# Kernel tuning notes

Hardware: AMD Instinct MI355X
Metric: run time of the kernel (lower is better)

Reference implementation:

```python
import jax, jax.numpy as jnp
import numpy as np

MARGIN = 1.0
N, D = 8192, 128
NUM_CLASSES = 1024


def setup_inputs() -> dict:
    key = jax.random.key(0)
    k1, k2, k3 = jax.random.split(key, 3)
    a = jax.random.normal(k1, (N, D), dtype=jnp.float32)
    b = jax.random.normal(k2, (N, D), dtype=jnp.float32)
    # L2-normalize embeddings (standard for metric learning; keeps exp() stable)
    a = a / jnp.linalg.norm(a, axis=1, keepdims=True)
    b = b / jnp.linalg.norm(b, axis=1, keepdims=True)
    labels = jax.random.randint(k3, (N,), 0, NUM_CLASSES, dtype=jnp.int64 if jax.config.jax_enable_x64 else jnp.int32)
    return {"a": a, "b": b, "labels": labels}


def reference(a, b, labels):
    # S[i, j] = a_i . b_j  -- full pairwise similarity, one GEMM
    S = a @ b.T  # [N, N]
    same = labels[:, None] == labels[None, :]  # [N, N]
    eye = jnp.eye(labels.shape[0], dtype=bool)
    pos_mask = same & ~eye          # ordered positive pairs (i != j, same label)
    neg_mask = ~same                # ordered negative pairs (labels differ)
    # V[i] = sum_k in neg(i) exp(margin + S[i, k])
    V = jnp.sum(jnp.where(neg_mask, jnp.exp(MARGIN + S), 0.0), axis=1)  # [N]
    # per positive pair (i, j): max(log(V_i + V_j) - S_ij, 0)^2
    hinge = jnp.maximum(jnp.log(V[:, None] + V[None, :]) - S, 0.0)
    comp = jnp.where(pos_mask, hinge * hinge, 0.0)
    num_pos = jnp.sum(pos_mask)
    loss = jnp.sum(comp) / (2.0 * num_pos.astype(S.dtype))
    return loss
```

## Files before the change

### kernel.cpp

```cpp
#include <hip/hip_runtime.h>

#define NN 8192
#define DD 128
#define MARGINF 1.0f
#define MAXCLS 64
#define NCHUNK 8
#define LOG2E 1.4426950408889634f
#define E1    2.718281828459045f

typedef __attribute__((ext_vector_type(8))) short bf16x8;
typedef __attribute__((ext_vector_type(4))) float f32x4;

#if __has_builtin(__builtin_amdgcn_exp2f)
#define EXP2F(x) __builtin_amdgcn_exp2f(x)
#else
#define EXP2F(x) exp2f(x)
#endif

__device__ __forceinline__ void load16_lds(const unsigned short* g, unsigned short* l) {
    __builtin_amdgcn_global_load_lds(
        (const __attribute__((address_space(1))) unsigned int*)g,
        (__attribute__((address_space(3))) unsigned int*)l,
        16, 0, 0);
}

__device__ __forceinline__ unsigned short f2bf(float x) {
    unsigned u = __float_as_uint(x);
    u = (u + 0x7FFFu + ((u >> 16) & 1u)) >> 16;
    return (unsigned short)u;
}

__global__ __launch_bounds__(256) void ml_convert_kernel(
    const float* __restrict__ a, const float* __restrict__ b,
    const int* __restrict__ labels,
    unsigned short* __restrict__ abf, unsigned short* __restrict__ bbf,
    int* __restrict__ cnt, int* __restrict__ list)
{
    int t = blockIdx.x * 256 + threadIdx.x;
    const float* src = a;
    unsigned short* dst = abf;
    int idx = t;
    float scale = LOG2E;
    if (t >= 262144) { src = b; dst = bbf; idx = t - 262144; scale = 1.0f; }
    float4 v = ((const float4*)src)[idx];
    ushort4 o;
    o.x = f2bf(v.x * scale); o.y = f2bf(v.y * scale);
    o.z = f2bf(v.z * scale); o.w = f2bf(v.w * scale);
    ((ushort4*)dst)[idx] = o;

    if (t < NN) {
        int c = labels[t];
        int p = atomicAdd(&cnt[c], 1);
        if (p < MAXCLS) list[c * MAXCLS + p] = t;
    }
}

__global__ __launch_bounds__(256, 2) void ml_vsum_gemm_kernel(
    const unsigned short* __restrict__ abf, const unsigned short* __restrict__ bbf,
    float* __restrict__ Vp)
{
    __shared__ unsigned short As[128 * DD];
    __shared__ unsigned short Bs[2][64 * DD];
    __shared__ float red[2][64];

    const int tid  = threadIdx.x;
    const int lane = tid & 63;
    const int wv   = tid >> 6;
    const int row0 = blockIdx.y * 128;
    const int j0   = blockIdx.x * 1024;

    const int lr = lane >> 4;
    const int p  = lane & 15;
    const int m  = lane & 15;
    const int q  = lane >> 4;
    const int xr = m & 7;

#pragma unroll
    for (int i = 0; i < 8; i++) {
        int rb = wv * 32 + i * 4;
        int r  = rb + lr;
        int cc = p ^ (r & 7);
        load16_lds(&abf[(size_t)(row0 + r) * DD + cc * 8], &As[rb * DD]);
    }
#pragma unroll
    for (int i = 0; i < 4; i++) {
        int rb = wv * 16 + i * 4;
        int r  = rb + lr;
        int cc = p ^ (r & 7);
        load16_lds(&bbf[(size_t)(j0 + r) * DD + cc * 8], &Bs[0][rb * DD]);
    }
#pragma unroll
    for (int i = 0; i < 4; i++) {
        int rb = wv * 16 + i * 4;
        int r  = rb + lr;
        int cc = p ^ (r & 7);
        load16_lds(&bbf[(size_t)(j0 + 64 + r) * DD + cc * 8], &Bs[1][rb * DD]);
    }
    __syncthreads();

    const int wi = (wv >> 1) * 64;
    const int wj = (wv & 1) * 32;

    bf16x8 afr[4][4];
#pragma unroll
    for (int ti = 0; ti < 4; ti++)
#pragma unroll
        for (int ks = 0; ks < 4; ks++) {
            int r   = wi + ti * 16 + m;
            int pos = (ks * 4 + q) ^ xr;
            afr[ti][ks] = *(const bf16x8*)(&As[r * DD + pos * 8]);
        }

    float rs[4][4];
#pragma unroll
    for (int ti = 0; ti < 4; ti++)
#pragma unroll
        for (int rg = 0; rg < 4; rg++) rs[ti][rg] = 0.f;

    const f32x4 zero = {0.f, 0.f, 0.f, 0.f};

#pragma unroll 2
    for (int jt = 0; jt < 16; jt++) {
        const int pb = jt & 1;
        f32x4 acc[4][2];
#pragma unroll
        for (int ti = 0; ti < 4; ti++)
#pragma unroll
            for (int tj = 0; tj < 2; tj++) acc[ti][tj] = zero;

#pragma unroll
        for (int ks = 0; ks < 4; ks++) {
            bf16x8 bfr[2];
#pragma unroll
            for (int tj = 0; tj < 2; tj++) {
                int r   = wj + tj * 16 + m;
                int pos = (ks * 4 + q) ^ xr;
                bfr[tj] = *(const bf16x8*)(&Bs[pb][r * DD + pos * 8]);
            }
#pragma unroll
            for (int ti = 0; ti < 4; ti++)
#pragma unroll
                for (int tj = 0; tj < 2; tj++)
                    acc[ti][tj] = __builtin_amdgcn_mfma_f32_16x16x32_bf16(afr[ti][ks], bfr[tj], acc[ti][tj], 0, 0, 0);
        }

#pragma unroll
        for (int ti = 0; ti < 4; ti++)
#pragma unroll
            for (int tj = 0; tj < 2; tj++) {
                f32x4 c = acc[ti][tj];
                rs[ti][0] += EXP2F(c[0]);
                rs[ti][1] += EXP2F(c[1]);
                rs[ti][2] += EXP2F(c[2]);
                rs[ti][3] += EXP2F(c[3]);
            }

        __syncthreads();
        if (jt < 14) {
            int jb = j0 + (jt + 2) * 64;
#pragma unroll
            for (int i = 0; i < 4; i++) {
                int rb = wv * 16 + i * 4;
                int r  = rb + lr;
                int cc = p ^ (r & 7);
                load16_lds(&bbf[(size_t)(jb + r) * DD + cc * 8], &Bs[pb][rb * DD]);
            }
        }
    }

#pragma unroll
    for (int ti = 0; ti < 4; ti++)
#pragma unroll
        for (int rg = 0; rg < 4; rg++) {
            float v = rs[ti][rg];
            v += __shfl_xor(v, 1);
            v += __shfl_xor(v, 2);
            v += __shfl_xor(v, 4);
            v += __shfl_xor(v, 8);
            rs[ti][rg] = v;
        }

    if ((wv & 1) == 1 && m == 0) {
#pragma unroll
        for (int ti = 0; ti < 4; ti++)
#pragma unroll
            for (int rg = 0; rg < 4; rg++)
                red[wv >> 1][ti * 16 + q * 4 + rg] = rs[ti][rg];
    }
    __syncthreads();
    if ((wv & 1) == 0 && m == 0) {
#pragma unroll
        for (int ti = 0; ti < 4; ti++)
#pragma unroll
            for (int rg = 0; rg < 4; rg++) {
                int rloc = ti * 16 + q * 4 + rg;
                Vp[(size_t)blockIdx.x * NN + row0 + wi + rloc] = rs[ti][rg] + red[wv >> 1][rloc];
            }
    }
}

__global__ __launch_bounds__(256) void ml_pairs_kernel(
    const float* __restrict__ a, const float* __restrict__ b,
    const int* __restrict__ cnt, const int* __restrict__ list,
    const float* __restrict__ Vp,
    float* __restrict__ classLoss, int* __restrict__ classCnt,
    unsigned int* __restrict__ done, float* __restrict__ out)
{
    __shared__ int   mem[MAXCLS];
    __shared__ float sumExp[MAXCLS];
    __shared__ float Vadj[MAXCLS];
    __shared__ float Sc[MAXCLS * MAXCLS];
    __shared__ float ps[4];
    __shared__ int   cs[4];
    __shared__ double dred[4];
    __shared__ long long cred[4];

    const int c   = blockIdx.x;
    const int tid = threadIdx.x;
    int mc = cnt[c];
    if (mc > MAXCLS) mc = MAXCLS;

    float vsum = 0.f;
    if (tid < mc) {
        int r = list[c * MAXCLS + tid];
        mem[tid] = r;
#pragma unroll
        for (int jc = 0; jc < NCHUNK; jc++) vsum += Vp[(size_t)jc * NN + r];
    }
    if (tid < MAXCLS) sumExp[tid] = 0.f;
    __syncthreads();

    const int g = tid >> 4;
    const int l = tid & 15;
    const int tot1 = mc * mc;
    for (int pp = g; pp < tot1; pp += 16) {
        int i = pp / mc;
        int j = pp - i * mc;
        int ri = mem[i], rj = mem[j];
        const float4* ar = (const float4*)(a + (size_t)ri * DD) + l * 2;
        const float4* br = (const float4*)(b + (size_t)rj * DD) + l * 2;
        float4 a0 = ar[0], a1 = ar[1];
        float4 b0 = br[0], b1 = br[1];
        float s = 0.f;
        s = fmaf(a0.x, b0.x, s); s = fmaf(a0.y, b0.y, s);
        s = fmaf(a0.z, b0.z, s); s = fmaf(a0.w, b0.w, s);
        s = fmaf(a1.x, b1.x, s); s = fmaf(a1.y, b1.y, s);
        s = fmaf(a1.z, b1.z, s); s = fmaf(a1.w, b1.w, s);
        s += __shfl_xor(s, 1);
        s += __shfl_xor(s, 2);
        s += __shfl_xor(s, 4);
        s += __shfl_xor(s, 8);
        if (l == 0) {
            Sc[i * MAXCLS + j] = s;
            atomicAdd(&sumExp[i], __expf(s));
        }
    }
    __syncthreads();

    if (tid < mc) Vadj[tid] = E1 * (vsum - sumExp[tid]);
    __syncthreads();

    float partial = 0.f;
    int   count   = 0;
    for (int pp = tid; pp < tot1; pp += 256) {
        int i = pp / mc;
        int j = pp - i * mc;
        if (i != j) {
            float h = fmaxf(logf(Vadj[i] + Vadj[j]) - Sc[i * MAXCLS + j], 0.f);
            partial += h * h;
            count++;
        }
    }
    for (int off = 32; off > 0; off >>= 1) {
        partial += __shfl_down(partial, off);
        count   += __shfl_down(count, off);
    }
    const int lane = tid & 63, wv = tid >> 6;
    if (lane == 0) { ps[wv] = partial; cs[wv] = count; }
    __syncthreads();

    if (tid == 0) {
        float tot = ps[0] + ps[1] + ps[2] + ps[3];
        int   ct  = cs[0] + cs[1] + cs[2] + cs[3];
        atomicExch(&classLoss[c], tot);
        atomicExch(&classCnt[c], ct);
    }
    __syncthreads();

    if (tid == 0) ps[0] = (float)atomicAdd(done, 1u);
    __syncthreads();
    if ((unsigned)ps[0] == 1023u) {
        double dls = 0.0;
        long long dct = 0;
        for (int k = tid; k < 1024; k += 256) {
            dls += (double)atomicAdd(&classLoss[k], 0.0f);
            dct += (long long)atomicAdd(&classCnt[k], 0);
        }
        for (int off = 32; off > 0; off >>= 1) {
            dls += __shfl_down(dls, off);
            dct += __shfl_down(dct, off);
        }
        if (lane == 0) { dred[wv] = dls; cred[wv] = dct; }
        __syncthreads();
        if (tid == 0) {
            double ls = dred[0] + dred[1] + dred[2] + dred[3];
            long long np = cred[0] + cred[1] + cred[2] + cred[3];
            out[0] = (float)(ls / (2.0 * (double)np));
        }
    }
}

extern "C" void kernel_launch(void* const* d_in, const int* in_sizes, int n_in,
                              void* d_out, int out_size, void* d_ws, size_t ws_size,
                              hipStream_t stream)
{
    const float* a      = (const float*)d_in[0];
    const float* b      = (const float*)d_in[1];
    const int*   labels = (const int*)d_in[2];
    float* out = (float*)d_out;

    char* ws = (char*)d_ws;
    unsigned short* abf = (unsigned short*)ws;
    unsigned short* bbf = (unsigned short*)(ws + 2097152);
    char*     base2     = ws + 4194304;
    int*      cnt       = (int*)(base2);
    unsigned* done      = (unsigned*)(base2 + 4096);
    float*    classLoss = (float*)(base2 + 8192);
    int*      classCnt  = (int*)(base2 + 12288);
    int*      list      = (int*)(base2 + 16384);
    float*    Vp        = (float*)(base2 + 278528);

    hipMemsetAsync(base2, 0, 4100, stream);

    ml_convert_kernel<<<2048, 256, 0, stream>>>(a, b, labels, abf, bbf, cnt, list);

    dim3 g(NCHUNK, NN / 128);
    ml_vsum_gemm_kernel<<<g, 256, 0, stream>>>(abf, bbf, Vp);

    ml_pairs_kernel<<<1024, 256, 0, stream>>>(a, b, cnt, list, Vp, classLoss, classCnt, done, out);
}
```

Measured before the change: 113.6 us.

## Fuse three kernels into one persistent kernel with grid barriers

Merges the convert, V-sum GEMM and per-class pair kernels into a single launch of 512 blocks, separated by software grid barriers built on atomics and fences. The shared-memory buffers of the phases are overlaid in a union, and each block handles two classes in the final phase. The goal is to remove the gaps and launch overhead between kernels. In exchange it depends on all 512 blocks being resident at once (two per CU), else the spin barrier deadlocks, and the pair phase now runs on half as many blocks.

```diff
diff --git a/kernel.cpp b/kernel.cpp
--- a/kernel.cpp
+++ b/kernel.cpp
@@ -2,9 +2,9 @@
 
 #define NN 8192
 #define DD 128
-#define MARGINF 1.0f
 #define MAXCLS 64
 #define NCHUNK 8
+#define GRID 512
 #define LOG2E 1.4426950408889634f
 #define E1    2.718281828459045f
 
@@ -17,6 +17,14 @@
 #define EXP2F(x) exp2f(x)
 #endif
 
+#if __has_builtin(__builtin_amdgcn_fence)
+#define FENCE_REL() __builtin_amdgcn_fence(__ATOMIC_RELEASE, "agent")
+#define FENCE_ACQ() __builtin_amdgcn_fence(__ATOMIC_ACQUIRE, "agent")
+#else
+#define FENCE_REL() __threadfence()
+#define FENCE_ACQ() __threadfence()
+#endif
+
 __device__ __forceinline__ void load16_lds(const unsigned short* g, unsigned short* l) {
     __builtin_amdgcn_global_load_lds(
         (const __attribute__((address_space(1))) unsigned int*)g,
@@ -30,266 +38,291 @@
     return (unsigned short)u;
 }
 
-__global__ __launch_bounds__(256) void ml_convert_kernel(
+__device__ __forceinline__ void grid_barrier(unsigned int* slot) {
+    FENCE_REL();
+    __syncthreads();
+    if (threadIdx.x == 0) {
+        atomicAdd(slot, 1u);
+        while (atomicAdd(slot, 0u) < (unsigned)GRID)
+            __builtin_amdgcn_s_sleep(2);
+    }
+    __syncthreads();
+    FENCE_ACQ();
+}
+
+__global__ __launch_bounds__(256, 2) void ml_mega_kernel(
     const float* __restrict__ a, const float* __restrict__ b,
     const int* __restrict__ labels,
     unsigned short* __restrict__ abf, unsigned short* __restrict__ bbf,
-    int* __restrict__ cnt, int* __restrict__ list)
+    int* __restrict__ cnt, int* __restrict__ list, float* __restrict__ Vp,
+    float* __restrict__ classLoss, int* __restrict__ classCnt,
+    unsigned int* __restrict__ bar, unsigned int* __restrict__ done,
+    float* __restrict__ out)
 {
-    int t = blockIdx.x * 256 + threadIdx.x;
-    const float* src = a;
-    unsigned short* dst = abf;
-    int idx = t;
-    float scale = LOG2E;
-    if (t >= 262144) { src = b; dst = bbf; idx = t - 262144; scale = 1.0f; }
-    float4 v = ((const float4*)src)[idx];
-    ushort4 o;
-    o.x = f2bf(v.x * scale); o.y = f2bf(v.y * scale);
-    o.z = f2bf(v.z * scale); o.w = f2bf(v.w * scale);
-    ((ushort4*)dst)[idx] = o;
-
-    if (t < NN) {
-        int c = labels[t];
-        int p = atomicAdd(&cnt[c], 1);
-        if (p < MAXCLS) list[c * MAXCLS + p] = t;
-    }
-}
-
-__global__ __launch_bounds__(256, 2) void ml_vsum_gemm_kernel(
-    const unsigned short* __restrict__ abf, const unsigned short* __restrict__ bbf,
-    float* __restrict__ Vp)
-{
-    __shared__ unsigned short As[128 * DD];
-    __shared__ unsigned short Bs[2][64 * DD];
-    __shared__ float red[2][64];
+    __shared__ union {
+        struct {
+            unsigned short As[128 * DD];
+            unsigned short Bs[2][64 * DD];
+            float red[2][64];
+        } g;
+        struct {
+            float Sc[MAXCLS * MAXCLS];
+            int   mem[MAXCLS];
+            float sumExp[MAXCLS];
+            float vadj[MAXCLS];
+            float ps[4];  int cs[4];
+            double dred[4];  long long cred[4];
+        } p;
+    } sh;
 
     const int tid  = threadIdx.x;
     const int lane = tid & 63;
     const int wv   = tid >> 6;
-    const int row0 = blockIdx.y * 128;
-    const int j0   = blockIdx.x * 1024;
-
-    const int lr = lane >> 4;
-    const int p  = lane & 15;
-    const int m  = lane & 15;
-    const int q  = lane >> 4;
-    const int xr = m & 7;
-
-#pragma unroll
-    for (int i = 0; i < 8; i++) {
-        int rb = wv * 32 + i * 4;
-        int r  = rb + lr;
-        int cc = p ^ (r & 7);
-        load16_lds(&abf[(size_t)(row0 + r) * DD + cc * 8], &As[rb * DD]);
-    }
-#pragma unroll
-    for (int i = 0; i < 4; i++) {
-        int rb = wv * 16 + i * 4;
-        int r  = rb + lr;
-        int cc = p ^ (r & 7);
-        load16_lds(&bbf[(size_t)(j0 + r) * DD + cc * 8], &Bs[0][rb * DD]);
-    }
-#pragma unroll
-    for (int i = 0; i < 4; i++) {
-        int rb = wv * 16 + i * 4;
-        int r  = rb + lr;
-        int cc = p ^ (r & 7);
-        load16_lds(&bbf[(size_t)(j0 + 64 + r) * DD + cc * 8], &Bs[1][rb * DD]);
+
+    {
+        const int gid = blockIdx.x * 256 + tid;
+#pragma unroll
+        for (int it = 0; it < 4; it++) {
+            int t = it * 131072 + gid;
+            const float* src = a;
+            unsigned short* dst = abf;
+            int idx = t;
+            float scale = LOG2E;
+            if (t >= 262144) { src = b; dst = bbf; idx = t - 262144; scale = 1.0f; }
+            float4 v = ((const float4*)src)[idx];
+            ushort4 o;
+            o.x = f2bf(v.x * scale); o.y = f2bf(v.y * scale);
+            o.z = f2bf(v.z * scale); o.w = f2bf(v.w * scale);
+            ((ushort4*)dst)[idx] = o;
+        }
+        if (gid < NN) {
+            int c = labels[gid];
+            int p0 = atomicAdd(&cnt[c], 1);
+            if (p0 < MAXCLS) list[c * MAXCLS + p0] = gid;
+        }
+    }
+
+    grid_barrier(&bar[0]);
+
+    {
+        const int row0 = (blockIdx.x & 63) * 128;
+        const int j0   = (blockIdx.x >> 6) * 1024;
+
+        const int lr = lane >> 4;
+        const int sp = lane & 15;
+        const int m  = lane & 15;
+        const int q  = lane >> 4;
+        const int xr = m & 7;
+
+#pragma unroll
+        for (int i = 0; i < 8; i++) {
+            int rb = wv * 32 + i * 4;
+            int r  = rb + lr;
+            int cc = sp ^ (r & 7);
+            load16_lds(&abf[(size_t)(row0 + r) * DD + cc * 8], &sh.g.As[rb * DD]);
+        }
+#pragma unroll
+        for (int i = 0; i < 4; i++) {
+            int rb = wv * 16 + i * 4;
+            int r  = rb + lr;
+            int cc = sp ^ (r & 7);
+            load16_lds(&bbf[(size_t)(j0 + r) * DD + cc * 8], &sh.g.Bs[0][rb * DD]);
+        }
+#pragma unroll
+        for (int i = 0; i < 4; i++) {
+            int rb = wv * 16 + i * 4;
+            int r  = rb + lr;
+            int cc = sp ^ (r & 7);
+            load16_lds(&bbf[(size_t)(j0 + 64 + r) * DD + cc * 8], &sh.g.Bs[1][rb * DD]);
+        }
+        __syncthreads();
+
+        const int wi = (wv >> 1) * 64;
+        const int wj = (wv & 1) * 32;
+
+        bf16x8 afr[4][4];
+#pragma unroll
+        for (int ti = 0; ti < 4; ti++)
+#pragma unroll
+            for (int ks = 0; ks < 4; ks++) {
+                int r   = wi + ti * 16 + m;
+                int pos = (ks * 4 + q) ^ xr;
+                afr[ti][ks] = *(const bf16x8*)(&sh.g.As[r * DD + pos * 8]);
+            }
+
+        float rs[4][4];
+#pragma unroll
+        for (int ti = 0; ti < 4; ti++)
+#pragma unroll
+            for (int rg = 0; rg < 4; rg++) rs[ti][rg] = 0.f;
+
+        const f32x4 zero = {0.f, 0.f, 0.f, 0.f};
+
+#pragma unroll 2
+        for (int jt = 0; jt < 16; jt++) {
+            const int pb = jt & 1;
+            f32x4 acc[4][2];
+#pragma unroll
+            for (int ti = 0; ti < 4; ti++)
+#pragma unroll
+                for (int tj = 0; tj < 2; tj++) acc[ti][tj] = zero;
+
+#pragma unroll
+            for (int ks = 0; ks < 4; ks++) {
+                bf16x8 bfr[2];
+#pragma unroll
+                for (int tj = 0; tj < 2; tj++) {
+                    int r   = wj + tj * 16 + m;
+                    int pos = (ks * 4 + q) ^ xr;
+                    bfr[tj] = *(const bf16x8*)(&sh.g.Bs[pb][r * DD + pos * 8]);
+                }
+#pragma unroll
+                for (int ti = 0; ti < 4; ti++)
+#pragma unroll
+                    for (int tj = 0; tj < 2; tj++)
+                        acc[ti][tj] = __builtin_amdgcn_mfma_f32_16x16x32_bf16(afr[ti][ks], bfr[tj], acc[ti][tj], 0, 0, 0);
+            }
+
+#pragma unroll
+            for (int ti = 0; ti < 4; ti++)
+#pragma unroll
+                for (int tj = 0; tj < 2; tj++) {
+                    f32x4 c = acc[ti][tj];
+                    rs[ti][0] += EXP2F(c[0]);
+                    rs[ti][1] += EXP2F(c[1]);
+                    rs[ti][2] += EXP2F(c[2]);
+                    rs[ti][3] += EXP2F(c[3]);
+                }
+
+            __syncthreads();
+            if (jt < 14) {
+                int jb = j0 + (jt + 2) * 64;
+#pragma unroll
+                for (int i = 0; i < 4; i++) {
+                    int rb = wv * 16 + i * 4;
+                    int r  = rb + lr;
+                    int cc = sp ^ (r & 7);
+                    load16_lds(&bbf[(size_t)(jb + r) * DD + cc * 8], &sh.g.Bs[pb][rb * DD]);
+                }
+            }
+        }
+
+#pragma unroll
+        for (int ti = 0; ti < 4; ti++)
+#pragma unroll
+            for (int rg = 0; rg < 4; rg++) {
+                float v = rs[ti][rg];
+                v += __shfl_xor(v, 1);
+                v += __shfl_xor(v, 2);
+                v += __shfl_xor(v, 4);
+                v += __shfl_xor(v, 8);
+                rs[ti][rg] = v;
+            }
+
+        if ((wv & 1) == 1 && m == 0) {
+#pragma unroll
+            for (int ti = 0; ti < 4; ti++)
+#pragma unroll
+                for (int rg = 0; rg < 4; rg++)
+                    sh.g.red[wv >> 1][ti * 16 + q * 4 + rg] = rs[ti][rg];
+        }
+        __syncthreads();
+        if ((wv & 1) == 0 && m == 0) {
+#pragma unroll
+            for (int ti = 0; ti < 4; ti++)
+#pragma unroll
+                for (int rg = 0; rg < 4; rg++) {
+                    int rloc = ti * 16 + q * 4 + rg;
+                    Vp[(size_t)(blockIdx.x >> 6) * NN + row0 + wi + rloc] = rs[ti][rg] + sh.g.red[wv >> 1][rloc];
+                }
+        }
+    }
+
+    grid_barrier(&bar[1]);
+
+    float blkLoss[2];
+    int   blkCnt[2];
+
+#pragma unroll 1
+    for (int rep = 0; rep < 2; rep++) {
+        const int c = blockIdx.x * 2 + rep;
+        __syncthreads();
+
+        int mc = cnt[c];
+        if (mc > MAXCLS) mc = MAXCLS;
+
+        float vsum = 0.f;
+        if (tid < mc) {
+            int r = list[c * MAXCLS + tid];
+            sh.p.mem[tid] = r;
+#pragma unroll
+            for (int jc = 0; jc < NCHUNK; jc++) vsum += Vp[(size_t)jc * NN + r];
+        }
+        if (tid < MAXCLS) sh.p.sumExp[tid] = 0.f;
+        __syncthreads();
+
+        const int g = tid >> 4;
+        const int l = tid & 15;
+        const int tot1 = mc * mc;
+        for (int pp = g; pp < tot1; pp += 16) {
+            int i = pp / mc;
+            int j = pp - i * mc;
+            int ri = sh.p.mem[i], rj = sh.p.mem[j];
+            const float4* ar = (const float4*)(a + (size_t)ri * DD) + l * 2;
+            const float4* br = (const float4*)(b + (size_t)rj * DD) + l * 2;
+            float4 a0 = ar[0], a1 = ar[1];
+            float4 b0 = br[0], b1 = br[1];
+            float s = 0.f;
+            s = fmaf(a0.x, b0.x, s); s = fmaf(a0.y, b0.y, s);
+            s = fmaf(a0.z, b0.z, s); s = fmaf(a0.w, b0.w, s);
+            s = fmaf(a1.x, b1.x, s); s = fmaf(a1.y, b1.y, s);
+            s = fmaf(a1.z, b1.z, s); s = fmaf(a1.w, b1.w, s);
+            s += __shfl_xor(s, 1);
+            s += __shfl_xor(s, 2);
+            s += __shfl_xor(s, 4);
+            s += __shfl_xor(s, 8);
+            if (l == 0) {
+                sh.p.Sc[i * MAXCLS + j] = s;
+                atomicAdd(&sh.p.sumExp[i], __expf(s));
+            }
+        }
+        __syncthreads();
+
+        if (tid < mc) sh.p.vadj[tid] = E1 * (vsum - sh.p.sumExp[tid]);
+        __syncthreads();
+
+        float partial = 0.f;
+        int   count   = 0;
+        for (int pp = tid; pp < tot1; pp += 256) {
+            int i = pp / mc;
+            int j = pp - i * mc;
+            if (i != j) {
+                float h = fmaxf(logf(sh.p.vadj[i] + sh.p.vadj[j]) - sh.p.Sc[i * MAXCLS + j], 0.f);
+                partial += h * h;
+                count++;
+            }
+        }
+        for (int off = 32; off > 0; off >>= 1) {
+            partial += __shfl_down(partial, off);
+            count   += __shfl_down(count, off);
+        }
+        if (lane == 0) { sh.p.ps[wv] = partial; sh.p.cs[wv] = count; }
+        __syncthreads();
+        blkLoss[rep] = sh.p.ps[0] + sh.p.ps[1] + sh.p.ps[2] + sh.p.ps[3];
+        blkCnt[rep]  = sh.p.cs[0] + sh.p.cs[1] + sh.p.cs[2] + sh.p.cs[3];
+    }
+
+    if (tid == 0) {
+        atomicExch(&classLoss[blockIdx.x * 2 + 0], blkLoss[0]);
+        atomicExch(&classCnt [blockIdx.x * 2 + 0], blkCnt[0]);
+        atomicExch(&classLoss[blockIdx.x * 2 + 1], blkLoss[1]);
+        atomicExch(&classCnt [blockIdx.x * 2 + 1], blkCnt[1]);
     }
     __syncthreads();
 
-    const int wi = (wv >> 1) * 64;
-    const int wj = (wv & 1) * 32;
-
-    bf16x8 afr[4][4];
-#pragma unroll
-    for (int ti = 0; ti < 4; ti++)
-#pragma unroll
-        for (int ks = 0; ks < 4; ks++) {
-            int r   = wi + ti * 16 + m;
-            int pos = (ks * 4 + q) ^ xr;
-            afr[ti][ks] = *(const bf16x8*)(&As[r * DD + pos * 8]);
-        }
-
-    float rs[4][4];
-#pragma unroll
-    for (int ti = 0; ti < 4; ti++)
-#pragma unroll
-        for (int rg = 0; rg < 4; rg++) rs[ti][rg] = 0.f;
-
-    const f32x4 zero = {0.f, 0.f, 0.f, 0.f};
-
-#pragma unroll 2
-    for (int jt = 0; jt < 16; jt++) {
-        const int pb = jt & 1;
-        f32x4 acc[4][2];
-#pragma unroll
-        for (int ti = 0; ti < 4; ti++)
-#pragma unroll
-            for (int tj = 0; tj < 2; tj++) acc[ti][tj] = zero;
-
-#pragma unroll
-        for (int ks = 0; ks < 4; ks++) {
-            bf16x8 bfr[2];
-#pragma unroll
-            for (int tj = 0; tj < 2; tj++) {
-                int r   = wj + tj * 16 + m;
-                int pos = (ks * 4 + q) ^ xr;
-                bfr[tj] = *(const bf16x8*)(&Bs[pb][r * DD + pos * 8]);
-            }
-#pragma unroll
-            for (int ti = 0; ti < 4; ti++)
-#pragma unroll
-                for (int tj = 0; tj < 2; tj++)
-                    acc[ti][tj] = __builtin_amdgcn_mfma_f32_16x16x32_bf16(afr[ti][ks], bfr[tj], acc[ti][tj], 0, 0, 0);
-        }
-
-#pragma unroll
-        for (int ti = 0; ti < 4; ti++)
-#pragma unroll
-            for (int tj = 0; tj < 2; tj++) {
-                f32x4 c = acc[ti][tj];
-                rs[ti][0] += EXP2F(c[0]);
-                rs[ti][1] += EXP2F(c[1]);
-                rs[ti][2] += EXP2F(c[2]);
-                rs[ti][3] += EXP2F(c[3]);
-            }
-
-        __syncthreads();
-        if (jt < 14) {
-            int jb = j0 + (jt + 2) * 64;
-#pragma unroll
-            for (int i = 0; i < 4; i++) {
-                int rb = wv * 16 + i * 4;
-                int r  = rb + lr;
-                int cc = p ^ (r & 7);
-                load16_lds(&bbf[(size_t)(jb + r) * DD + cc * 8], &Bs[pb][rb * DD]);
-            }
-        }
-    }
-
-#pragma unroll
-    for (int ti = 0; ti < 4; ti++)
-#pragma unroll
-        for (int rg = 0; rg < 4; rg++) {
-            float v = rs[ti][rg];
-            v += __shfl_xor(v, 1);
-            v += __shfl_xor(v, 2);
-            v += __shfl_xor(v, 4);
-            v += __shfl_xor(v, 8);
-            rs[ti][rg] = v;
-        }
-
-    if ((wv & 1) == 1 && m == 0) {
-#pragma unroll
-        for (int ti = 0; ti < 4; ti++)
-#pragma unroll
-            for (int rg = 0; rg < 4; rg++)
-                red[wv >> 1][ti * 16 + q * 4 + rg] = rs[ti][rg];
-    }
+    if (tid == 0) sh.p.ps[0] = (float)atomicAdd(done, 1u);
     __syncthreads();
-    if ((wv & 1) == 0 && m == 0) {
-#pragma unroll
-        for (int ti = 0; ti < 4; ti++)
-#pragma unroll
-            for (int rg = 0; rg < 4; rg++) {
-                int rloc = ti * 16 + q * 4 + rg;
-                Vp[(size_t)blockIdx.x * NN + row0 + wi + rloc] = rs[ti][rg] + red[wv >> 1][rloc];
-            }
-    }
-}
-
-__global__ __launch_bounds__(256) void ml_pairs_kernel(
-    const float* __restrict__ a, const float* __restrict__ b,
-    const int* __restrict__ cnt, const int* __restrict__ list,
-    const float* __restrict__ Vp,
-    float* __restrict__ classLoss, int* __restrict__ classCnt,
-    unsigned int* __restrict__ done, float* __restrict__ out)
-{
-    __shared__ int   mem[MAXCLS];
-    __shared__ float sumExp[MAXCLS];
-    __shared__ float Vadj[MAXCLS];
-    __shared__ float Sc[MAXCLS * MAXCLS];
-    __shared__ float ps[4];
-    __shared__ int   cs[4];
-    __shared__ double dred[4];
-    __shared__ long long cred[4];
-
-    const int c   = blockIdx.x;
-    const int tid = threadIdx.x;
-    int mc = cnt[c];
-    if (mc > MAXCLS) mc = MAXCLS;
-
-    float vsum = 0.f;
-    if (tid < mc) {
-        int r = list[c * MAXCLS + tid];
-        mem[tid] = r;
-#pragma unroll
-        for (int jc = 0; jc < NCHUNK; jc++) vsum += Vp[(size_t)jc * NN + r];
-    }
-    if (tid < MAXCLS) sumExp[tid] = 0.f;
-    __syncthreads();
-
-    const int g = tid >> 4;
-    const int l = tid & 15;
-    const int tot1 = mc * mc;
-    for (int pp = g; pp < tot1; pp += 16) {
-        int i = pp / mc;
-        int j = pp - i * mc;
-        int ri = mem[i], rj = mem[j];
-        const float4* ar = (const float4*)(a + (size_t)ri * DD) + l * 2;
-        const float4* br = (const float4*)(b + (size_t)rj * DD) + l * 2;
-        float4 a0 = ar[0], a1 = ar[1];
-        float4 b0 = br[0], b1 = br[1];
-        float s = 0.f;
-        s = fmaf(a0.x, b0.x, s); s = fmaf(a0.y, b0.y, s);
-        s = fmaf(a0.z, b0.z, s); s = fmaf(a0.w, b0.w, s);
-        s = fmaf(a1.x, b1.x, s); s = fmaf(a1.y, b1.y, s);
-        s = fmaf(a1.z, b1.z, s); s = fmaf(a1.w, b1.w, s);
-        s += __shfl_xor(s, 1);
-        s += __shfl_xor(s, 2);
-        s += __shfl_xor(s, 4);
-        s += __shfl_xor(s, 8);
-        if (l == 0) {
-            Sc[i * MAXCLS + j] = s;
-            atomicAdd(&sumExp[i], __expf(s));
-        }
-    }
-    __syncthreads();
-
-    if (tid < mc) Vadj[tid] = E1 * (vsum - sumExp[tid]);
-    __syncthreads();
-
-    float partial = 0.f;
-    int   count   = 0;
-    for (int pp = tid; pp < tot1; pp += 256) {
-        int i = pp / mc;
-        int j = pp - i * mc;
-        if (i != j) {
-            float h = fmaxf(logf(Vadj[i] + Vadj[j]) - Sc[i * MAXCLS + j], 0.f);
-            partial += h * h;
-            count++;
-        }
-    }
-    for (int off = 32; off > 0; off >>= 1) {
-        partial += __shfl_down(partial, off);
-        count   += __shfl_down(count, off);
-    }
-    const int lane = tid & 63, wv = tid >> 6;
-    if (lane == 0) { ps[wv] = partial; cs[wv] = count; }
-    __syncthreads();
-
-    if (tid == 0) {
-        float tot = ps[0] + ps[1] + ps[2] + ps[3];
-        int   ct  = cs[0] + cs[1] + cs[2] + cs[3];
-        atomicExch(&classLoss[c], tot);
-        atomicExch(&classCnt[c], ct);
-    }
-    __syncthreads();
-
-    if (tid == 0) ps[0] = (float)atomicAdd(done, 1u);
-    __syncthreads();
-    if ((unsigned)ps[0] == 1023u) {
+    if ((unsigned)sh.p.ps[0] == (unsigned)(GRID - 1)) {
         double dls = 0.0;
         long long dct = 0;
         for (int k = tid; k < 1024; k += 256) {
@@ -300,11 +333,11 @@
             dls += __shfl_down(dls, off);
             dct += __shfl_down(dct, off);
         }
-        if (lane == 0) { dred[wv] = dls; cred[wv] = dct; }
+        if (lane == 0) { sh.p.dred[wv] = dls; sh.p.cred[wv] = dct; }
         __syncthreads();
         if (tid == 0) {
-            double ls = dred[0] + dred[1] + dred[2] + dred[3];
-            long long np = cred[0] + cred[1] + cred[2] + cred[3];
+            double ls = sh.p.dred[0] + sh.p.dred[1] + sh.p.dred[2] + sh.p.dred[3];
+            long long np = sh.p.cred[0] + sh.p.cred[1] + sh.p.cred[2] + sh.p.cred[3];
             out[0] = (float)(ls / (2.0 * (double)np));
         }
     }
@@ -324,18 +357,16 @@
     unsigned short* bbf = (unsigned short*)(ws + 2097152);
     char*     base2     = ws + 4194304;
     int*      cnt       = (int*)(base2);
-    unsigned* done      = (unsigned*)(base2 + 4096);
+    unsigned* bar       = (unsigned*)(base2 + 4096);
+    unsigned* done      = (unsigned*)(base2 + 4112);
     float*    classLoss = (float*)(base2 + 8192);
     int*      classCnt  = (int*)(base2 + 12288);
     int*      list      = (int*)(base2 + 16384);
     float*    Vp        = (float*)(base2 + 278528);
 
-    hipMemsetAsync(base2, 0, 4100, stream);
-
-    ml_convert_kernel<<<2048, 256, 0, stream>>>(a, b, labels, abf, bbf, cnt, list);
-
-    dim3 g(NCHUNK, NN / 128);
-    ml_vsum_gemm_kernel<<<g, 256, 0, stream>>>(abf, bbf, Vp);
-
-    ml_pairs_kernel<<<1024, 256, 0, stream>>>(a, b, cnt, list, Vp, classLoss, classCnt, done, out);
-}
+    (void)hipMemsetAsync(base2, 0, 4128, stream);
+
+    ml_mega_kernel<<<GRID, 256, 0, stream>>>(a, b, labels, abf, bbf,
+                                             cnt, list, Vp, classLoss, classCnt,
+                                             bar, done, out);
+}
```

Result: slower. 251.2 us (+121.0%).
